# Kernel optimization log

Hardware: AMD Instinct MI355X
Metric: run time of the kernel (lower is better)

## Reference

```python
import jax, jax.numpy as jnp
import numpy as np
import math

P = 2
TAU = 1.0
USE_POW = False
ALIGN_W = 1.0
ENTROPY_W = 1.0
EPS = 1e-12


def _pairwise_l2(z):
    # torch.cdist(z, z, p=2): sqrt of squared distances via GEMM decomposition
    sq = jnp.sum(z * z, axis=-1)  # [N]
    d2 = sq[:, None] + sq[None, :] - 2.0 * (z @ z.T)  # [N, N]
    d = jnp.sqrt(jnp.maximum(d2, 0.0))
    return jnp.maximum(d, EPS)  # clamp_min(eps)


def setup_inputs() -> dict:
    key = jax.random.key(0)
    k0, k1 = jax.random.split(key)
    v0 = jax.random.normal(k0, (8192, 256), dtype=jnp.float32)
    v1 = jax.random.normal(k1, (8192, 256), dtype=jnp.float32)
    return {"v0": v0, "v1": v1}


def reference(v0, v1):
    views = [v0, v1]
    n = v0.shape[0]

    # Alignment term: mean Lp distance between matched rows, one pair (0,1)
    diff = v0 - v1
    align = jnp.sqrt(jnp.sum(diff * diff, axis=-1)).mean()  # p=2 norm per row

    # Entropy term: masked logsumexp over within-view pairwise distances
    log_num_neg = math.log(n - 1)
    eye = jnp.eye(n, dtype=bool)
    entropy = jnp.float32(0.0)
    for z in views:
        dist = _pairwise_l2(z)  # [N, N]
        logits = jnp.where(eye, -jnp.inf, -dist / TAU)
        lme = jax.nn.logsumexp(logits, axis=1) - log_num_neg  # [N]
        entropy = entropy + lme.mean()
    entropy = entropy / len(views)

    return ALIGN_W * align + ENTROPY_W * entropy
```

## Files before the change

kernel.cpp:

```cpp
#include <hip/hip_runtime.h>
#include <math.h>


#define D_DIM 256
#define NB 64
#define NBLK 2080
#define S_Q 26.0f
#define LOG2E2 2.0813689810f

typedef int i32x4 __attribute__((ext_vector_type(4)));
typedef unsigned int u32;
#define AS1 __attribute__((address_space(1)))
#define AS3 __attribute__((address_space(3)))

__device__ inline void load_lds16(const void* g, void* l) {
  __builtin_amdgcn_global_load_lds((const AS1 u32*)g, (AS3 u32*)l, 16, 0, 0);
}

__device__ inline int q8(float x) {
  return __float2int_rn(fminf(fmaxf(x * S_Q, -127.0f), 127.0f));
}
__device__ inline u32 q8x4(const float4 f) {
  return (u32)(q8(f.x) & 255) | ((u32)(q8(f.y) & 255) << 8) |
         ((u32)(q8(f.z) & 255) << 16) | ((u32)(q8(f.w) & 255) << 24);
}

__global__ __launch_bounds__(256) void prep(
    const float* __restrict__ v0, const float* __restrict__ v1,
    unsigned char* __restrict__ ph0, unsigned char* __restrict__ ph1,
    float* __restrict__ sq0, float* __restrict__ sq1,
    float* __restrict__ S0, float* __restrict__ S1,
    float* __restrict__ align_part) {
  __shared__ float4 l0[1024], l1[1024];
  __shared__ float red0[4][16], red1[4][16], red2[4][16];
  const int R = blockIdx.x;
  const int t = threadIdx.x;

  #pragma unroll
  for (int p = 0; p < 4; ++p) {
    const int slot = t + p * 256;
    const size_t g = (size_t)(R * 16 + (slot >> 6)) * 64 + (slot & 63);
    l0[slot] = ((const float4*)v0)[g];
    l1[slot] = ((const float4*)v1)[g];
  }
  __syncthreads();

  {
    const int rr = t & 15, c = t >> 4;
    const int s = c >> 2, q = c & 3;
    const int li = rr * 64 + c * 4;
    uint4 u0, u1;
    u0.x = q8x4(l0[li + 0]); u0.y = q8x4(l0[li + 1]);
    u0.z = q8x4(l0[li + 2]); u0.w = q8x4(l0[li + 3]);
    u1.x = q8x4(l1[li + 0]); u1.y = q8x4(l1[li + 1]);
    u1.z = q8x4(l1[li + 2]); u1.w = q8x4(l1[li + 3]);
    const size_t dst = (size_t)(R * 4 + s) * 64 + q * 16 + rr;
    ((uint4*)ph0)[dst] = u0;
    ((uint4*)ph1)[dst] = u1;
  }

  {
    const int rr = t & 15;
    const int base = rr * 64 + (t >> 4) * 4;
    float s0p = 0.f, s1p = 0.f, s2p = 0.f;
    #pragma unroll
    for (int c = 0; c < 4; ++c) {
      const float4 a = l0[base + c], b = l1[base + c];
      s0p += a.x * a.x + a.y * a.y + a.z * a.z + a.w * a.w;
      s1p += b.x * b.x + b.y * b.y + b.z * b.z + b.w * b.w;
      const float dx = a.x - b.x, dy = a.y - b.y, dz = a.z - b.z, dw = a.w - b.w;
      s2p += dx * dx + dy * dy + dz * dz + dw * dw;
    }
    s0p += __shfl_xor(s0p, 16, 64); s0p += __shfl_xor(s0p, 32, 64);
    s1p += __shfl_xor(s1p, 16, 64); s1p += __shfl_xor(s1p, 32, 64);
    s2p += __shfl_xor(s2p, 16, 64); s2p += __shfl_xor(s2p, 32, 64);
    const int w = t >> 6, lane = t & 63;
    if (lane < 16) { red0[w][lane] = s0p; red1[w][lane] = s1p; red2[w][lane] = s2p; }
  }
  __syncthreads();
  if (t < 16) {
    const int row = R * 16 + t;
    const float a0 = red0[0][t] + red0[1][t] + red0[2][t] + red0[3][t];
    const float a1 = red1[0][t] + red1[1][t] + red1[2][t] + red1[3][t];
    const float a2 = red2[0][t] + red2[1][t] + red2[2][t] + red2[3][t];
    sq0[row] = a0 * LOG2E2;
    sq1[row] = a1 * LOG2E2;
    align_part[row] = sqrtf(a2);
    S0[row] = 0.0f;
    S1[row] = 0.0f;
  }
}

__global__ __launch_bounds__(256) void entropy_tile(
    const unsigned char* __restrict__ ph0, const unsigned char* __restrict__ ph1,
    const float* __restrict__ sq0, const float* __restrict__ sq1,
    float* __restrict__ S0, float* __restrict__ S1) {
  const unsigned char* __restrict__ ph = blockIdx.y ? ph1 : ph0;
  const float* __restrict__ sq = blockIdx.y ? sq1 : sq0;
  float* __restrict__ S        = blockIdx.y ? S1 : S0;

  const int b = blockIdx.x;
  int bi = (int)((129.0 - sqrt(16641.0 - 8.0 * (double)b)) * 0.5);
  while ((bi + 1) * NB - ((bi + 1) * bi) / 2 <= b) ++bi;
  while (bi * NB - (bi * (bi - 1)) / 2 > b) --bi;
  const int bj = bi + (b - (bi * NB - (bi * (bi - 1)) / 2));
  const bool diag = (bi == bj);

  __shared__ __align__(16) char smem[32768];
  float* swp = (float*)smem;

  const int t = threadIdx.x, lane = t & 63, w = t >> 6;
  const int wi = w >> 1, wj = w & 1;
  const int quad = lane >> 4, l15 = lane & 15;
  const int i0 = bi * 128, j0 = bj * 128;

  #pragma unroll
  for (int r8 = 0; r8 < 8; ++r8) {
    const int seg = w * 8 + r8;
    const unsigned char* src = ph + (size_t)bi * 32768 + seg * 1024 + lane * 16;
    load_lds16(src, smem + seg * 1024);
  }

  const i32x4* __restrict__ phv = (const i32x4*)ph;
  const int baseB = ((bj * 8 + wj * 4) * 4) * 64 + lane;

  i32x4 bF[2][4];
  #pragma unroll
  for (int n = 0; n < 4; ++n) bF[0][n] = phv[baseB + (n * 4) * 64];

  i32x4 acc[4][4];
  #pragma unroll
  for (int m = 0; m < 4; ++m)
    #pragma unroll
    for (int n = 0; n < 4; ++n)
      acc[m][n] = (i32x4){0, 0, 0, 0};

  __syncthreads();

  const i32x4* smemv = (const i32x4*)smem;
  #pragma unroll
  for (int s = 0; s < 4; ++s) {
    const int cur = s & 1, nxt = cur ^ 1;
    if (s < 3) {
      #pragma unroll
      for (int n = 0; n < 4; ++n)
        bF[nxt][n] = phv[baseB + (n * 4 + s + 1) * 64];
    }
    i32x4 ah[4];
    #pragma unroll
    for (int m = 0; m < 4; ++m)
      ah[m] = smemv[(size_t)((wi * 4 + m) * 4 + s) * 64 + lane];
    #pragma unroll
    for (int m = 0; m < 4; ++m)
      #pragma unroll
      for (int n = 0; n < 4; ++n)
        acc[m][n] = __builtin_amdgcn_mfma_i32_16x16x64_i8(ah[m], bF[cur][n], acc[m][n], 0, 0, 0);
  }

  __syncthreads();

  const float K2 = 2.0f * LOG2E2 / (S_Q * S_Q);
  float sj[4];
  #pragma unroll
  for (int n = 0; n < 4; ++n) sj[n] = sq[j0 + wj * 64 + n * 16 + l15];

  const int wbase = w * 1088;
  float csum[4] = {0.f, 0.f, 0.f, 0.f};
  #pragma unroll
  for (int m = 0; m < 4; ++m) {
    #pragma unroll
    for (int r = 0; r < 4; ++r) {
      const int rowl = m * 16 + quad * 4 + r;
      const int gi = i0 + wi * 64 + rowl;
      const float si = sq[gi];
      float p = 0.f;
      #pragma unroll
      for (int n = 0; n < 4; ++n) {
        const float d2 = fmaxf(fmaf(-K2, (float)acc[m][n][r], si + sj[n]), 0.0f);
        const float dist = __builtin_amdgcn_sqrtf(d2);
        float e = __builtin_amdgcn_exp2f(-dist);
        if (diag && gi == j0 + wj * 64 + n * 16 + l15) e = 0.f;
        p += e;
        csum[n] += e;
      }
      swp[wbase + rowl * 17 + l15] = p;
    }
  }
  {
    float rs = 0.f;
    #pragma unroll
    for (int j = 0; j < 16; ++j) rs += swp[wbase + lane * 17 + j];
    atomicAdd(&S[i0 + wi * 64 + lane], rs);
  }
  if (!diag) {
    #pragma unroll
    for (int n = 0; n < 4; ++n) {
      float c2 = csum[n];
      c2 += __shfl_xor(c2, 16, 64);
      c2 += __shfl_xor(c2, 32, 64);
      if (quad == 0) atomicAdd(&S[j0 + wj * 64 + n * 16 + l15], c2);
    }
  }
}

__global__ __launch_bounds__(256) void finalize_part(
    const float* __restrict__ S0, const float* __restrict__ S1,
    const float* __restrict__ align_part,
    float* __restrict__ part_log, float* __restrict__ part_align) {
  __shared__ float shl[4], sha[4];
  const int t = threadIdx.x, lane = t & 63, w = t >> 6;
  const int idx = blockIdx.x * 256 + t;
  float lg = __logf(S0[idx]) + __logf(S1[idx]);
  float al = align_part[idx];
  #pragma unroll
  for (int o = 1; o < 64; o <<= 1) {
    lg += __shfl_xor(lg, o, 64);
    al += __shfl_xor(al, o, 64);
  }
  if (lane == 0) { shl[w] = lg; sha[w] = al; }
  __syncthreads();
  if (t == 0) {
    part_log[blockIdx.x] = shl[0] + shl[1] + shl[2] + shl[3];
    part_align[blockIdx.x] = sha[0] + sha[1] + sha[2] + sha[3];
  }
}

__global__ void finalize_final(const float* __restrict__ part_log,
                               const float* __restrict__ part_align,
                               float* __restrict__ out, int n) {
  const int lane = threadIdx.x & 63;
  double lg = (lane < 32) ? (double)part_log[lane] : 0.0;
  double al = (lane < 32) ? (double)part_align[lane] : 0.0;
  #pragma unroll
  for (int o = 1; o < 32; o <<= 1) {
    lg += __shfl_xor(lg, o, 64);
    al += __shfl_xor(al, o, 64);
  }
  if (lane == 0) {
    double align = al / (double)n;
    double entropy = 0.5 * lg / (double)n - log((double)(n - 1));
    out[0] = (float)(align + entropy);
  }
}

extern "C" void kernel_launch(void* const* d_in, const int* in_sizes, int n_in,
                              void* d_out, int out_size, void* d_ws, size_t ws_size,
                              hipStream_t stream) {
  const float* v0 = (const float*)d_in[0];
  const float* v1 = (const float*)d_in[1];
  float* out = (float*)d_out;
  const int n = in_sizes[0] / D_DIM;

  float* ws         = (float*)d_ws;
  float* sq0        = ws;
  float* sq1        = ws + n;
  float* S0         = ws + 2 * n;
  float* S1         = ws + 3 * n;
  float* align_part = ws + 4 * n;
  float* part_log   = ws + 5 * n;
  float* part_align = ws + 5 * n + 32;
  unsigned char* ph0 = (unsigned char*)(ws + 5 * n + 64);
  unsigned char* ph1 = ph0 + (size_t)n * D_DIM;

  prep<<<n / 16, 256, 0, stream>>>(v0, v1, ph0, ph1, sq0, sq1, S0, S1, align_part);

  dim3 grid(NBLK, 2);
  entropy_tile<<<grid, 256, 0, stream>>>(ph0, ph1, sq0, sq1, S0, S1);

  finalize_part<<<n / 256, 256, 0, stream>>>(S0, S1, align_part, part_log, part_align);
  finalize_final<<<1, 64, 0, stream>>>(part_log, part_align, out, n);
}
```

Baseline: 120.2 us.

## Swizzle tile order across XCDs, pad prep LDS, hoist sq loads, drop clamp

Flattens the entropy grid into one dimension and remaps block IDs so consecutive blocks on each XCD walk the triangular tile space in column order, improving L2 reuse of the shared B panel. Pads the prep kernel's LDS rows to 65 float4 to reduce bank conflicts, prefetches the column squared-norms before the MFMA loop, and removes the max(d2,0) clamp. Dropping the clamp risks NaN if quantized d2 goes negative off the diagonal.

```diff
diff --git a/kernel.cpp b/kernel.cpp
--- a/kernel.cpp
+++ b/kernel.cpp
@@ -7,6 +7,7 @@
 #define NBLK 2080
 #define S_Q 26.0f
 #define LOG2E2 2.0813689810f
+#define LP 65
 
 typedef int i32x4 __attribute__((ext_vector_type(4)));
 typedef unsigned int u32;
@@ -31,7 +32,7 @@
     float* __restrict__ sq0, float* __restrict__ sq1,
     float* __restrict__ S0, float* __restrict__ S1,
     float* __restrict__ align_part) {
-  __shared__ float4 l0[1024], l1[1024];
+  __shared__ float4 l0[16 * LP], l1[16 * LP];
   __shared__ float red0[4][16], red1[4][16], red2[4][16];
   const int R = blockIdx.x;
   const int t = threadIdx.x;
@@ -39,16 +40,17 @@
   #pragma unroll
   for (int p = 0; p < 4; ++p) {
     const int slot = t + p * 256;
-    const size_t g = (size_t)(R * 16 + (slot >> 6)) * 64 + (slot & 63);
-    l0[slot] = ((const float4*)v0)[g];
-    l1[slot] = ((const float4*)v1)[g];
+    const int r = slot >> 6, col = slot & 63;
+    const size_t g = (size_t)(R * 16 + r) * 64 + col;
+    l0[r * LP + col] = ((const float4*)v0)[g];
+    l1[r * LP + col] = ((const float4*)v1)[g];
   }
   __syncthreads();
 
   {
     const int rr = t & 15, c = t >> 4;
     const int s = c >> 2, q = c & 3;
-    const int li = rr * 64 + c * 4;
+    const int li = rr * LP + c * 4;
     uint4 u0, u1;
     u0.x = q8x4(l0[li + 0]); u0.y = q8x4(l0[li + 1]);
     u0.z = q8x4(l0[li + 2]); u0.w = q8x4(l0[li + 3]);
@@ -61,7 +63,7 @@
 
   {
     const int rr = t & 15;
-    const int base = rr * 64 + (t >> 4) * 4;
+    const int base = rr * LP + (t >> 4) * 4;
     float s0p = 0.f, s1p = 0.f, s2p = 0.f;
     #pragma unroll
     for (int c = 0; c < 4; ++c) {
@@ -95,15 +97,19 @@
     const unsigned char* __restrict__ ph0, const unsigned char* __restrict__ ph1,
     const float* __restrict__ sq0, const float* __restrict__ sq1,
     float* __restrict__ S0, float* __restrict__ S1) {
-  const unsigned char* __restrict__ ph = blockIdx.y ? ph1 : ph0;
-  const float* __restrict__ sq = blockIdx.y ? sq1 : sq0;
-  float* __restrict__ S        = blockIdx.y ? S1 : S0;
-
-  const int b = blockIdx.x;
-  int bi = (int)((129.0 - sqrt(16641.0 - 8.0 * (double)b)) * 0.5);
-  while ((bi + 1) * NB - ((bi + 1) * bi) / 2 <= b) ++bi;
-  while (bi * NB - (bi * (bi - 1)) / 2 > b) --bi;
-  const int bj = bi + (b - (bi * NB - (bi * (bi - 1)) / 2));
+  const int u = blockIdx.x;
+  const int lin2 = (u & 7) * (2 * NBLK / 8) + (u >> 3);
+  const int view = lin2 >= NBLK;
+  const int lin = view ? lin2 - NBLK : lin2;
+
+  const unsigned char* __restrict__ ph = view ? ph1 : ph0;
+  const float* __restrict__ sq = view ? sq1 : sq0;
+  float* __restrict__ S        = view ? S1 : S0;
+
+  int bj = (int)((sqrt(8.0 * (double)lin + 1.0) - 1.0) * 0.5);
+  while ((bj + 1) * (bj + 2) / 2 <= lin) ++bj;
+  while (bj * (bj + 1) / 2 > lin) --bj;
+  const int bi = lin - bj * (bj + 1) / 2;
   const bool diag = (bi == bj);
 
   __shared__ __align__(16) char smem[32768];
@@ -134,6 +140,10 @@
     #pragma unroll
     for (int n = 0; n < 4; ++n)
       acc[m][n] = (i32x4){0, 0, 0, 0};
+
+  float sj[4];
+  #pragma unroll
+  for (int n = 0; n < 4; ++n) sj[n] = sq[j0 + wj * 64 + n * 16 + l15];
 
   __syncthreads();
 
@@ -160,11 +170,8 @@
   __syncthreads();
 
   const float K2 = 2.0f * LOG2E2 / (S_Q * S_Q);
-  float sj[4];
-  #pragma unroll
-  for (int n = 0; n < 4; ++n) sj[n] = sq[j0 + wj * 64 + n * 16 + l15];
-
   const int wbase = w * 1088;
+
   float csum[4] = {0.f, 0.f, 0.f, 0.f};
   #pragma unroll
   for (int m = 0; m < 4; ++m) {
@@ -176,9 +183,8 @@
       float p = 0.f;
       #pragma unroll
       for (int n = 0; n < 4; ++n) {
-        const float d2 = fmaxf(fmaf(-K2, (float)acc[m][n][r], si + sj[n]), 0.0f);
-        const float dist = __builtin_amdgcn_sqrtf(d2);
-        float e = __builtin_amdgcn_exp2f(-dist);
+        const float d2 = fmaf(-K2, (float)acc[m][n][r], si + sj[n]);
+        float e = __builtin_amdgcn_exp2f(-__builtin_amdgcn_sqrtf(d2));
         if (diag && gi == j0 + wj * 64 + n * 16 + l15) e = 0.f;
         p += e;
         csum[n] += e;
@@ -264,8 +270,7 @@
 
   prep<<<n / 16, 256, 0, stream>>>(v0, v1, ph0, ph1, sq0, sq1, S0, S1, align_part);
 
-  dim3 grid(NBLK, 2);
-  entropy_tile<<<grid, 256, 0, stream>>>(ph0, ph1, sq0, sq1, S0, S1);
+  entropy_tile<<<2 * NBLK, 256, 0, stream>>>(ph0, ph1, sq0, sq1, S0, S1);
 
   finalize_part<<<n / 256, 256, 0, stream>>>(S0, S1, align_part, part_log, part_align);
   finalize_final<<<1, 64, 0, stream>>>(part_log, part_align, out, n);
```

After: 121.9 us. No clear change (+1.4%).
